# Optimization experiments

Measured on AMD Instinct MI355X. Metric: run time of the kernel, lower is better.

## Reference

```python
import jax, jax.numpy as jnp
import numpy as np

N, E, D = 50000, 800000, 128
BN_EPS = 1e-5


def setup_inputs() -> dict:
    key = jax.random.key(0)
    ks = jax.random.split(key, 6)
    x = jax.random.normal(ks[0], (N, D), dtype=jnp.float32)
    edge_index = jax.random.randint(ks[1], (2, E), 0, N, dtype=jnp.int32)
    edge_attr = jax.random.normal(ks[2], (E, D), dtype=jnp.float32)
    sc = 1.0 / np.sqrt(D).astype(np.float32)
    W1 = jax.random.normal(ks[3], (D, D), dtype=jnp.float32) * sc
    b1 = jnp.zeros((D,), jnp.float32)
    W2 = jax.random.normal(ks[4], (D, D), dtype=jnp.float32) * sc
    b2 = jnp.zeros((D,), jnp.float32)
    bn_w = jnp.ones((D,), jnp.float32)
    bn_b = jnp.zeros((D,), jnp.float32)
    return dict(x=x, edge_index=edge_index, edge_attr=edge_attr,
                W1=W1, b1=b1, W2=W2, b2=b2, bn_w=bn_w, bn_b=bn_b)


def reference(x, edge_index, edge_attr, W1, b1, W2, b2, bn_w, bn_b):
    # GINEConv: aggr_i = sum_{j->i} ReLU(x_j + e_ji); out = MLP((1+eps)*x + aggr), eps=0
    src, dst = edge_index[0], edge_index[1]
    msg = jax.nn.relu(x[src] + edge_attr)                     # [E, D] gather + elementwise
    aggr = jax.ops.segment_sum(msg, dst, num_segments=x.shape[0])  # scatter-add -> [N, D]
    h = x + aggr                                              # (1 + eps) * x, eps = 0
    h = jax.nn.relu(h @ W1 + b1) @ W2 + b2                    # GIN 2-layer MLP
    h = x + h                                                 # dropout(p=0) + residual
    # BatchNorm1d (training-mode batch statistics, biased variance)
    mean = jnp.mean(h, axis=0)
    var = jnp.var(h, axis=0)
    h = (h - mean) * jax.lax.rsqrt(var + BN_EPS) * bn_w + bn_b
    return h
```

## Files before the change

### kernel.cpp

```cpp
#include <hip/hip_runtime.h>
#include <stdint.h>

#define BN_EPS 1e-5f
#define WPAD 136

typedef short s8v __attribute__((ext_vector_type(8)));
typedef float f4v __attribute__((ext_vector_type(4)));

__device__ __forceinline__ float b2f(uint16_t h){
    uint32_t u = ((uint32_t)h) << 16; float f; __builtin_memcpy(&f, &u, 4); return f;
}
__device__ __forceinline__ uint16_t f2b(float f){
    uint32_t u; __builtin_memcpy(&u, &f, 4);
    uint32_t r = (u + 0x7fffu + ((u >> 16) & 1u)) >> 16;
    return (uint16_t)r;
}
__device__ __forceinline__ float lo16(uint32_t v){ return b2f((uint16_t)(v & 0xffffu)); }
__device__ __forceinline__ float hi16(uint32_t v){ return b2f((uint16_t)(v >> 16)); }
__device__ __forceinline__ uint32_t pack2(float a, float b){
    return (uint32_t)f2b(a) | ((uint32_t)f2b(b) << 16);
}

__global__ void k_detect(const uint32_t* __restrict__ xb, int* __restrict__ flag){
    int tid = threadIdx.x;
    uint32_t w = xb[tid];
    float v; __builtin_memcpy(&v, &w, 4);
    float a = fabsf(v);
    bool plaus = (v == 0.0f) || (a > 1e-6f && a < 1e6f);
    unsigned long long m = __ballot(plaus);
    if (tid == 0) flag[0] = (__popcll(m) >= 48) ? 1 : 0;
}

__global__ __launch_bounds__(256) void k_prep(const void* __restrict__ W1, const void* __restrict__ W2,
                                              const void* __restrict__ b1, const void* __restrict__ b2,
                                              const void* __restrict__ bnw, const void* __restrict__ bnb,
                                              const int* __restrict__ flag,
                                              uint16_t* __restrict__ WT1c, uint16_t* __restrict__ WT2c,
                                              float* __restrict__ vecs){
    bool f32 = flag[0] != 0;
    int i = blockIdx.x * 256 + threadIdx.x;
    if (i < 16384){
        int k = i >> 7, n = i & 127;
        float w1 = f32 ? ((const float*)W1)[i] : b2f(((const uint16_t*)W1)[i]);
        float w2 = f32 ? ((const float*)W2)[i] : b2f(((const uint16_t*)W2)[i]);
        WT1c[n * 128 + k] = f2b(w1);
        WT2c[n * 128 + k] = f2b(w2);
    }
    if (i < 128){
        vecs[i]       = f32 ? ((const float*)b1)[i]  : b2f(((const uint16_t*)b1)[i]);
        vecs[128 + i] = f32 ? ((const float*)b2)[i]  : b2f(((const uint16_t*)b2)[i]);
        vecs[256 + i] = f32 ? ((const float*)bnw)[i] : b2f(((const uint16_t*)bnw)[i]);
        vecs[384 + i] = f32 ? ((const float*)bnb)[i] : b2f(((const uint16_t*)bnb)[i]);
    }
}

__global__ void k_hist(const int* __restrict__ dst, int* __restrict__ counts, int E){
    int e = blockIdx.x * 256 + threadIdx.x;
    if (e < E){
        int d = dst[e];
        if (d >= 0) atomicAdd(&counts[d], 1);
    }
}

__global__ __launch_bounds__(1024) void k_scan(int* __restrict__ counts, int* __restrict__ cursor, int N){
    const int T = 1024;
    int tid = threadIdx.x;
    int chunk = (N + T - 1) / T;
    int beg = tid * chunk;
    int end = beg + chunk; if (end > N) end = N;
    int s = 0;
    for (int i = beg; i < end; ++i) s += counts[i];
    __shared__ int sm[T];
    sm[tid] = s; __syncthreads();
    for (int off = 1; off < T; off <<= 1){
        int v = (tid >= off) ? sm[tid - off] : 0;
        __syncthreads();
        sm[tid] += v;
        __syncthreads();
    }
    int run = sm[tid] - s;
    for (int i = beg; i < end; ++i){
        int c = counts[i];
        counts[i] = run; cursor[i] = run;
        run += c;
    }
    if (tid == T - 1){ counts[N] = run; cursor[N] = run; }
}

__global__ void k_scatter(const int* __restrict__ dst, int* __restrict__ cursor,
                          int* __restrict__ perm, int E){
    int e = blockIdx.x * 256 + threadIdx.x;
    if (e < E){
        int d = dst[e];
        if (d >= 0){
            int p = atomicAdd(&cursor[d], 1);
            if (p >= 0 && p < E) perm[p] = e;
        }
    }
}

__global__ __launch_bounds__(256) void k_agg(const void* __restrict__ x,
                                             const void* __restrict__ ea,
                                             const int* __restrict__ src,
                                             const int* __restrict__ offs,
                                             const int* __restrict__ perm,
                                             const int* __restrict__ flag,
                                             uint32_t* __restrict__ h0_2, int N, int E){
    int node = (blockIdx.x << 2) + (threadIdx.x >> 6);
    int lane = threadIdx.x & 63;
    if (node >= N) return;
    bool f32 = flag[0] != 0;
    int beg = offs[node], end = offs[node + 1];
    if (beg < 0) beg = 0;
    if (end > E) end = E;
    float a0 = 0.f, a1 = 0.f;
    if (f32){
        const float2* xf = (const float2*)x;
        const float2* ef = (const float2*)ea;
        for (int p = beg; p < end; ++p){
            int e = perm[p];
            e = e < 0 ? 0 : (e >= E ? E - 1 : e);
            int s = src[e];
            s = s < 0 ? 0 : (s >= N ? N - 1 : s);
            float2 xv = xf[(size_t)s * 64 + lane];
            float2 ev = ef[(size_t)e * 64 + lane];
            a0 += fmaxf(xv.x + ev.x, 0.f);
            a1 += fmaxf(xv.y + ev.y, 0.f);
        }
        float2 xn = xf[(size_t)node * 64 + lane];
        a0 += xn.x; a1 += xn.y;
    } else {
        const uint32_t* x2 = (const uint32_t*)x;
        const uint32_t* e2 = (const uint32_t*)ea;
        for (int p = beg; p < end; ++p){
            int e = perm[p];
            e = e < 0 ? 0 : (e >= E ? E - 1 : e);
            int s = src[e];
            s = s < 0 ? 0 : (s >= N ? N - 1 : s);
            uint32_t xv = x2[(size_t)s * 64 + lane];
            uint32_t ev = e2[(size_t)e * 64 + lane];
            a0 += fmaxf(lo16(xv) + lo16(ev), 0.f);
            a1 += fmaxf(hi16(xv) + hi16(ev), 0.f);
        }
        uint32_t xn = x2[(size_t)node * 64 + lane];
        a0 += lo16(xn); a1 += hi16(xn);
    }
    h0_2[(size_t)node * 64 + lane] = pack2(a0, a1);
}

__global__ __launch_bounds__(256) void k_mlp(const uint16_t* __restrict__ h0,
                                             const uint16_t* __restrict__ WT1,
                                             const uint16_t* __restrict__ WT2,
                                             const float* __restrict__ vecs,
                                             uint16_t* __restrict__ h2out, int N){
    __shared__ uint16_t Ws[128 * WPAD];
    __shared__ uint16_t H1[64 * WPAD];
    int tid = threadIdx.x;
    int lane = tid & 63;
    int w = tid >> 6;
    int r0 = blockIdx.x * 64;
    int mrow = lane & 15;
    int quad = lane >> 4;

    {
        const uint32_t* g = (const uint32_t*)WT1;
        #pragma unroll
        for (int j = 0; j < 32; ++j){
            int u = tid + 256 * j;
            int el = u << 1; int r = el >> 7, c = el & 127;
            *(uint32_t*)&Ws[r * WPAD + c] = g[u];
        }
    }
    __syncthreads();

    int arow = r0 + (w << 4) + mrow;
    int arow_c = arow < N ? arow : N - 1;
    s8v a[4];
    #pragma unroll
    for (int kt = 0; kt < 4; ++kt)
        a[kt] = *(const s8v*)(h0 + (size_t)arow_c * 128 + kt * 32 + quad * 8);

    #pragma unroll
    for (int nt = 0; nt < 8; ++nt){
        f4v acc = {0.f, 0.f, 0.f, 0.f};
        #pragma unroll
        for (int kt = 0; kt < 4; ++kt){
            s8v b = *(const s8v*)&Ws[(nt * 16 + mrow) * WPAD + kt * 32 + quad * 8];
            acc = __builtin_amdgcn_mfma_f32_16x16x32_bf16(a[kt], b, acc, 0, 0, 0);
        }
        int col = nt * 16 + mrow;
        float bias = vecs[col];
        #pragma unroll
        for (int r = 0; r < 4; ++r){
            float v = fmaxf(acc[r] + bias, 0.f);
            int lrow = (w << 4) + quad * 4 + r;
            H1[lrow * WPAD + col] = f2b(v);
        }
    }
    __syncthreads();

    {
        const uint32_t* g = (const uint32_t*)WT2;
        #pragma unroll
        for (int j = 0; j < 32; ++j){
            int u = tid + 256 * j;
            int el = u << 1; int r = el >> 7, c = el & 127;
            *(uint32_t*)&Ws[r * WPAD + c] = g[u];
        }
    }
    __syncthreads();

    s8v a2[4];
    #pragma unroll
    for (int kt = 0; kt < 4; ++kt)
        a2[kt] = *(const s8v*)&H1[((w << 4) + mrow) * WPAD + kt * 32 + quad * 8];

    #pragma unroll
    for (int nt = 0; nt < 8; ++nt){
        f4v acc = {0.f, 0.f, 0.f, 0.f};
        #pragma unroll
        for (int kt = 0; kt < 4; ++kt){
            s8v b = *(const s8v*)&Ws[(nt * 16 + mrow) * WPAD + kt * 32 + quad * 8];
            acc = __builtin_amdgcn_mfma_f32_16x16x32_bf16(a2[kt], b, acc, 0, 0, 0);
        }
        int col = nt * 16 + mrow;
        float bias = vecs[128 + col];
        #pragma unroll
        for (int r = 0; r < 4; ++r){
            int grow = r0 + (w << 4) + quad * 4 + r;
            if (grow < N)
                h2out[(size_t)grow * 128 + col] = f2b(acc[r] + bias);
        }
    }
}

__global__ __launch_bounds__(256) void k_stats(const uint32_t* __restrict__ h2_2,
                                               const void* __restrict__ x,
                                               const int* __restrict__ flag,
                                               float* __restrict__ ssum,
                                               float* __restrict__ ssq, int N){
    bool f32 = flag[0] != 0;
    int tid = threadIdx.x;
    int cp = tid & 63;
    int rl = tid >> 6;
    int rbase = blockIdx.x * 256;
    int rend = rbase + 256; if (rend > N) rend = N;
    float s0 = 0.f, s1 = 0.f, q0 = 0.f, q1 = 0.f;
    for (int r = rbase + rl; r < rend; r += 4){
        uint32_t hv = h2_2[(size_t)r * 64 + cp];
        float x0, x1;
        if (f32){ float2 xv = ((const float2*)x)[(size_t)r * 64 + cp]; x0 = xv.x; x1 = xv.y; }
        else    { uint32_t xv = ((const uint32_t*)x)[(size_t)r * 64 + cp]; x0 = lo16(xv); x1 = hi16(xv); }
        float f0 = lo16(hv) + x0;
        float f1 = hi16(hv) + x1;
        s0 += f0; q0 += f0 * f0;
        s1 += f1; q1 += f1 * f1;
    }
    __shared__ float R[4][256];
    R[0][tid] = s0; R[1][tid] = s1; R[2][tid] = q0; R[3][tid] = q1;
    __syncthreads();
    if (tid < 64){
        for (int g = 1; g < 4; ++g){
            s0 += R[0][tid + 64 * g]; s1 += R[1][tid + 64 * g];
            q0 += R[2][tid + 64 * g]; q1 += R[3][tid + 64 * g];
        }
        atomicAdd(&ssum[2 * tid],     s0);
        atomicAdd(&ssum[2 * tid + 1], s1);
        atomicAdd(&ssq[2 * tid],      q0);
        atomicAdd(&ssq[2 * tid + 1],  q1);
    }
}

__global__ __launch_bounds__(256) void k_norm(void* __restrict__ out,
                                              const uint32_t* __restrict__ h2_2,
                                              const void* __restrict__ x,
                                              const int* __restrict__ flag,
                                              const float* __restrict__ ssum,
                                              const float* __restrict__ ssq,
                                              const float* __restrict__ vecs,
                                              int N, int total2){
    __shared__ float sc[128], sh[128];
    bool f32 = flag[0] != 0;
    int tid = threadIdx.x;
    if (tid < 128){
        float invN = 1.f / (float)N;
        float mean = ssum[tid] * invN;
        float var = ssq[tid] * invN - mean * mean;
        var = fmaxf(var, 0.f);
        float s = vecs[256 + tid] * rsqrtf(var + BN_EPS);
        sc[tid] = s;
        sh[tid] = vecs[384 + tid] - mean * s;
    }
    __syncthreads();
    for (int i = blockIdx.x * 256 + tid; i < total2; i += gridDim.x * 256){
        uint32_t hv = h2_2[i];
        float x0, x1;
        if (f32){ float2 xv = ((const float2*)x)[i]; x0 = xv.x; x1 = xv.y; }
        else    { uint32_t xv = ((const uint32_t*)x)[i]; x0 = lo16(xv); x1 = hi16(xv); }
        int cp = i & 63;
        float f0 = (lo16(hv) + x0) * sc[2 * cp]     + sh[2 * cp];
        float f1 = (hi16(hv) + x1) * sc[2 * cp + 1] + sh[2 * cp + 1];
        if (f32){ float2 o; o.x = f0; o.y = f1; ((float2*)out)[i] = o; }
        else    { ((uint32_t*)out)[i] = pack2(f0, f1); }
    }
}

extern "C" void kernel_launch(void* const* d_in, const int* in_sizes, int n_in,
                              void* d_out, int out_size, void* d_ws, size_t ws_size,
                              hipStream_t stream){
    const void* x   = d_in[0];
    const int*  ei  = (const int*)d_in[1];
    const void* ea  = d_in[2];
    const void* W1  = d_in[3];
    const void* b1  = d_in[4];
    const void* W2  = d_in[5];
    const void* b2  = d_in[6];
    const void* bnw = d_in[7];
    const void* bnb = d_in[8];

    int N = in_sizes[0] / 128;
    int E = in_sizes[1] / 2;
    const int* src = ei;
    const int* dst = ei + E;

    char* ws = (char*)d_ws;
    size_t off = 0;
    auto alloc = [&](size_t bytes){ size_t o = off; off += (bytes + 255) & ~(size_t)255; return o; };
    size_t o_counts = alloc((size_t)(N + 1) * 4);
    size_t o_cursor = alloc((size_t)(N + 1) * 4);
    size_t o_stats  = alloc(256 * 4);
    size_t o_flag   = alloc(4);
    size_t zeroBytes = off;
    size_t o_wt1  = alloc(16384 * 2);
    size_t o_wt2  = alloc(16384 * 2);
    size_t o_vecs = alloc(512 * 4);
    size_t o_h2   = alloc((size_t)N * 128 * 2);
    size_t o_perm = alloc((size_t)E * 4);

    int E_used = E;
    if (off > ws_size){
        size_t fixed = o_perm;
        size_t avail = ws_size > fixed ? ws_size - fixed : 0;
        long long cap = (long long)(avail / 4);
        if (cap < E_used) E_used = (int)(cap < 0 ? 0 : cap);
    }

    int* counts = (int*)(ws + o_counts);
    int* cursor = (int*)(ws + o_cursor);
    float* ssum = (float*)(ws + o_stats);
    float* ssq  = ssum + 128;
    int* flag   = (int*)(ws + o_flag);
    uint16_t* WT1 = (uint16_t*)(ws + o_wt1);
    uint16_t* WT2 = (uint16_t*)(ws + o_wt2);
    float* vecs = (float*)(ws + o_vecs);
    uint16_t* h2 = (uint16_t*)(ws + o_h2);
    int* perm   = (int*)(ws + o_perm);
    uint16_t* h0 = (uint16_t*)d_out;

    hipMemsetAsync(d_ws, 0, zeroBytes, stream);

    k_detect<<<1, 64, 0, stream>>>((const uint32_t*)x, flag);
    k_hist<<<(E_used + 255) / 256, 256, 0, stream>>>(dst, counts, E_used);
    k_scan<<<1, 1024, 0, stream>>>(counts, cursor, N);
    k_scatter<<<(E_used + 255) / 256, 256, 0, stream>>>(dst, cursor, perm, E_used);
    k_prep<<<64, 256, 0, stream>>>(W1, W2, b1, b2, bnw, bnb, flag, WT1, WT2, vecs);
    k_agg<<<(N + 3) / 4, 256, 0, stream>>>(x, ea, src, counts, perm, flag,
                                           (uint32_t*)h0, N, E_used);
    k_mlp<<<(N + 63) / 64, 256, 0, stream>>>(h0, WT1, WT2, vecs, h2, N);
    k_stats<<<(N + 255) / 256, 256, 0, stream>>>((const uint32_t*)h2, x, flag, ssum, ssq, N);
    k_norm<<<2048, 256, 0, stream>>>(d_out, (const uint32_t*)h2, x, flag, ssum, ssq,
                                     vecs, N, N * 64);
}
```

Before: 926.6 us.

## Pack edge/src pairs, batch-load indices in agg, fuse BN stats into MLP

The scatter kernel now writes (edge, src) pairs, so aggregation no longer needs a dependent src lookup. Each wave loads 64 pairs at once and broadcasts them with shuffles, unrolled by four to keep more gathers in flight. The MLP kernel now adds the residual, writes h3 in fp32 and accumulates the BatchNorm sums in shared memory, which removes the separate stats kernel. The cost is an fp32 intermediate that doubles h3 traffic, plus the MLP reading x itself.

```diff
diff --git a/kernel.cpp b/kernel.cpp
--- a/kernel.cpp
+++ b/kernel.cpp
@@ -54,11 +54,11 @@
     }
 }
 
-__global__ void k_hist(const int* __restrict__ dst, int* __restrict__ counts, int E){
+__global__ void k_hist(const int* __restrict__ dst, int* __restrict__ counts, int N, int E){
     int e = blockIdx.x * 256 + threadIdx.x;
     if (e < E){
         int d = dst[e];
-        if (d >= 0) atomicAdd(&counts[d], 1);
+        if (d >= 0 && d < N) atomicAdd(&counts[d], 1);
     }
 }
 
@@ -87,23 +87,25 @@
     if (tid == T - 1){ counts[N] = run; cursor[N] = run; }
 }
 
-__global__ void k_scatter(const int* __restrict__ dst, int* __restrict__ cursor,
-                          int* __restrict__ perm, int E){
+__global__ void k_scatter(const int* __restrict__ dst, const int* __restrict__ src,
+                          int* __restrict__ cursor, int2* __restrict__ pe, int N, int E){
     int e = blockIdx.x * 256 + threadIdx.x;
     if (e < E){
         int d = dst[e];
-        if (d >= 0){
+        if (d >= 0 && d < N){
             int p = atomicAdd(&cursor[d], 1);
-            if (p >= 0 && p < E) perm[p] = e;
+            if (p >= 0 && p < E){
+                int2 v; v.x = e; v.y = src[e];
+                pe[p] = v;
+            }
         }
     }
 }
 
 __global__ __launch_bounds__(256) void k_agg(const void* __restrict__ x,
                                              const void* __restrict__ ea,
-                                             const int* __restrict__ src,
+                                             const int2* __restrict__ pe,
                                              const int* __restrict__ offs,
-                                             const int* __restrict__ perm,
                                              const int* __restrict__ flag,
                                              uint32_t* __restrict__ h0_2, int N, int E){
     int node = (blockIdx.x << 2) + (threadIdx.x >> 6);
@@ -114,35 +116,75 @@
     if (beg < 0) beg = 0;
     if (end > E) end = E;
     float a0 = 0.f, a1 = 0.f;
+
+    const float2* xf = (const float2*)x;
+    const float2* ef = (const float2*)ea;
+    const uint32_t* xh = (const uint32_t*)x;
+    const uint32_t* eh = (const uint32_t*)ea;
+
+    for (int cb = beg; cb < end; cb += 64){
+        int idx = cb + lane;
+        int2 p;
+        if (idx < end) p = pe[idx]; else { p.x = 0; p.y = 0; }
+        int e = p.x, s = p.y;
+        e = e < 0 ? 0 : (e >= E ? E - 1 : e);
+        s = s < 0 ? 0 : (s >= N ? N - 1 : s);
+        int m = end - cb; if (m > 64) m = 64;
+
+        if (f32){
+            int i = 0;
+            for (; i + 4 <= m; i += 4){
+                int e0 = __shfl(e, i),     s0 = __shfl(s, i);
+                int e1 = __shfl(e, i + 1), s1 = __shfl(s, i + 1);
+                int e2 = __shfl(e, i + 2), s2 = __shfl(s, i + 2);
+                int e3 = __shfl(e, i + 3), s3 = __shfl(s, i + 3);
+                float2 x0 = xf[(size_t)s0 * 64 + lane], v0 = ef[(size_t)e0 * 64 + lane];
+                float2 x1 = xf[(size_t)s1 * 64 + lane], v1 = ef[(size_t)e1 * 64 + lane];
+                float2 x2 = xf[(size_t)s2 * 64 + lane], v2 = ef[(size_t)e2 * 64 + lane];
+                float2 x3 = xf[(size_t)s3 * 64 + lane], v3 = ef[(size_t)e3 * 64 + lane];
+                a0 += fmaxf(x0.x + v0.x, 0.f); a1 += fmaxf(x0.y + v0.y, 0.f);
+                a0 += fmaxf(x1.x + v1.x, 0.f); a1 += fmaxf(x1.y + v1.y, 0.f);
+                a0 += fmaxf(x2.x + v2.x, 0.f); a1 += fmaxf(x2.y + v2.y, 0.f);
+                a0 += fmaxf(x3.x + v3.x, 0.f); a1 += fmaxf(x3.y + v3.y, 0.f);
+            }
+            for (; i < m; ++i){
+                int ei = __shfl(e, i), si = __shfl(s, i);
+                float2 xv = xf[(size_t)si * 64 + lane];
+                float2 ev = ef[(size_t)ei * 64 + lane];
+                a0 += fmaxf(xv.x + ev.x, 0.f);
+                a1 += fmaxf(xv.y + ev.y, 0.f);
+            }
+        } else {
+            int i = 0;
+            for (; i + 4 <= m; i += 4){
+                int e0 = __shfl(e, i),     s0 = __shfl(s, i);
+                int e1 = __shfl(e, i + 1), s1 = __shfl(s, i + 1);
+                int e2 = __shfl(e, i + 2), s2 = __shfl(s, i + 2);
+                int e3 = __shfl(e, i + 3), s3 = __shfl(s, i + 3);
+                uint32_t x0 = xh[(size_t)s0 * 64 + lane], v0 = eh[(size_t)e0 * 64 + lane];
+                uint32_t x1 = xh[(size_t)s1 * 64 + lane], v1 = eh[(size_t)e1 * 64 + lane];
+                uint32_t x2 = xh[(size_t)s2 * 64 + lane], v2 = eh[(size_t)e2 * 64 + lane];
+                uint32_t x3 = xh[(size_t)s3 * 64 + lane], v3 = eh[(size_t)e3 * 64 + lane];
+                a0 += fmaxf(lo16(x0) + lo16(v0), 0.f); a1 += fmaxf(hi16(x0) + hi16(v0), 0.f);
+                a0 += fmaxf(lo16(x1) + lo16(v1), 0.f); a1 += fmaxf(hi16(x1) + hi16(v1), 0.f);
+                a0 += fmaxf(lo16(x2) + lo16(v2), 0.f); a1 += fmaxf(hi16(x2) + hi16(v2), 0.f);
+                a0 += fmaxf(lo16(x3) + lo16(v3), 0.f); a1 += fmaxf(hi16(x3) + hi16(v3), 0.f);
+            }
+            for (; i < m; ++i){
+                int ei = __shfl(e, i), si = __shfl(s, i);
+                uint32_t xv = xh[(size_t)si * 64 + lane];
+                uint32_t ev = eh[(size_t)ei * 64 + lane];
+                a0 += fmaxf(lo16(xv) + lo16(ev), 0.f);
+                a1 += fmaxf(hi16(xv) + hi16(ev), 0.f);
+            }
+        }
+    }
+
     if (f32){
-        const float2* xf = (const float2*)x;
-        const float2* ef = (const float2*)ea;
-        for (int p = beg; p < end; ++p){
-            int e = perm[p];
-            e = e < 0 ? 0 : (e >= E ? E - 1 : e);
-            int s = src[e];
-            s = s < 0 ? 0 : (s >= N ? N - 1 : s);
-            float2 xv = xf[(size_t)s * 64 + lane];
-            float2 ev = ef[(size_t)e * 64 + lane];
-            a0 += fmaxf(xv.x + ev.x, 0.f);
-            a1 += fmaxf(xv.y + ev.y, 0.f);
-        }
         float2 xn = xf[(size_t)node * 64 + lane];
         a0 += xn.x; a1 += xn.y;
     } else {
-        const uint32_t* x2 = (const uint32_t*)x;
-        const uint32_t* e2 = (const uint32_t*)ea;
-        for (int p = beg; p < end; ++p){
-            int e = perm[p];
-            e = e < 0 ? 0 : (e >= E ? E - 1 : e);
-            int s = src[e];
-            s = s < 0 ? 0 : (s >= N ? N - 1 : s);
-            uint32_t xv = x2[(size_t)s * 64 + lane];
-            uint32_t ev = e2[(size_t)e * 64 + lane];
-            a0 += fmaxf(lo16(xv) + lo16(ev), 0.f);
-            a1 += fmaxf(hi16(xv) + hi16(ev), 0.f);
-        }
-        uint32_t xn = x2[(size_t)node * 64 + lane];
+        uint32_t xn = xh[(size_t)node * 64 + lane];
         a0 += lo16(xn); a1 += hi16(xn);
     }
     h0_2[(size_t)node * 64 + lane] = pack2(a0, a1);
@@ -152,9 +194,15 @@
                                              const uint16_t* __restrict__ WT1,
                                              const uint16_t* __restrict__ WT2,
                                              const float* __restrict__ vecs,
-                                             uint16_t* __restrict__ h2out, int N){
+                                             const void* __restrict__ x,
+                                             const int* __restrict__ flag,
+                                             float* __restrict__ h3out,
+                                             float* __restrict__ ssum,
+                                             float* __restrict__ ssq, int N){
     __shared__ uint16_t Ws[128 * WPAD];
     __shared__ uint16_t H1[64 * WPAD];
+    __shared__ float lsum[128], lsq[128];
+    bool xf32 = flag[0] != 0;
     int tid = threadIdx.x;
     int lane = tid & 63;
     int w = tid >> 6;
@@ -162,6 +210,8 @@
     int mrow = lane & 15;
     int quad = lane >> 4;
 
+    if (tid < 128){ lsum[tid] = 0.f; lsq[tid] = 0.f; }
+
     {
         const uint32_t* g = (const uint32_t*)WT1;
         #pragma unroll
@@ -215,6 +265,9 @@
     for (int kt = 0; kt < 4; ++kt)
         a2[kt] = *(const s8v*)&H1[((w << 4) + mrow) * WPAD + kt * 32 + quad * 8];
 
+    const float* xf = (const float*)x;
+    const uint16_t* xh = (const uint16_t*)x;
+
     #pragma unroll
     for (int nt = 0; nt < 8; ++nt){
         f4v acc = {0.f, 0.f, 0.f, 0.f};
@@ -225,55 +278,36 @@
         }
         int col = nt * 16 + mrow;
         float bias = vecs[128 + col];
+        float s_part = 0.f, q_part = 0.f;
         #pragma unroll
         for (int r = 0; r < 4; ++r){
             int grow = r0 + (w << 4) + quad * 4 + r;
-            if (grow < N)
-                h2out[(size_t)grow * 128 + col] = f2b(acc[r] + bias);
-        }
-    }
-}
-
-__global__ __launch_bounds__(256) void k_stats(const uint32_t* __restrict__ h2_2,
-                                               const void* __restrict__ x,
-                                               const int* __restrict__ flag,
-                                               float* __restrict__ ssum,
-                                               float* __restrict__ ssq, int N){
-    bool f32 = flag[0] != 0;
-    int tid = threadIdx.x;
-    int cp = tid & 63;
-    int rl = tid >> 6;
-    int rbase = blockIdx.x * 256;
-    int rend = rbase + 256; if (rend > N) rend = N;
-    float s0 = 0.f, s1 = 0.f, q0 = 0.f, q1 = 0.f;
-    for (int r = rbase + rl; r < rend; r += 4){
-        uint32_t hv = h2_2[(size_t)r * 64 + cp];
-        float x0, x1;
-        if (f32){ float2 xv = ((const float2*)x)[(size_t)r * 64 + cp]; x0 = xv.x; x1 = xv.y; }
-        else    { uint32_t xv = ((const uint32_t*)x)[(size_t)r * 64 + cp]; x0 = lo16(xv); x1 = hi16(xv); }
-        float f0 = lo16(hv) + x0;
-        float f1 = hi16(hv) + x1;
-        s0 += f0; q0 += f0 * f0;
-        s1 += f1; q1 += f1 * f1;
-    }
-    __shared__ float R[4][256];
-    R[0][tid] = s0; R[1][tid] = s1; R[2][tid] = q0; R[3][tid] = q1;
+            if (grow < N){
+                float xv = xf32 ? xf[(size_t)grow * 128 + col]
+                                : b2f(xh[(size_t)grow * 128 + col]);
+                float h3 = xv + acc[r] + bias;
+                h3out[(size_t)grow * 128 + col] = h3;
+                s_part += h3; q_part += h3 * h3;
+            }
+        }
+        float sr = s_part + __shfl_xor(s_part, 16);
+        sr += __shfl_xor(sr, 32);
+        float qr = q_part + __shfl_xor(q_part, 16);
+        qr += __shfl_xor(qr, 32);
+        if (quad == 0){
+            atomicAdd(&lsum[col], sr);
+            atomicAdd(&lsq[col], qr);
+        }
+    }
     __syncthreads();
-    if (tid < 64){
-        for (int g = 1; g < 4; ++g){
-            s0 += R[0][tid + 64 * g]; s1 += R[1][tid + 64 * g];
-            q0 += R[2][tid + 64 * g]; q1 += R[3][tid + 64 * g];
-        }
-        atomicAdd(&ssum[2 * tid],     s0);
-        atomicAdd(&ssum[2 * tid + 1], s1);
-        atomicAdd(&ssq[2 * tid],      q0);
-        atomicAdd(&ssq[2 * tid + 1],  q1);
+    if (tid < 128){
+        atomicAdd(&ssum[tid], lsum[tid]);
+        atomicAdd(&ssq[tid], lsq[tid]);
     }
 }
 
 __global__ __launch_bounds__(256) void k_norm(void* __restrict__ out,
-                                              const uint32_t* __restrict__ h2_2,
-                                              const void* __restrict__ x,
+                                              const float2* __restrict__ h3,
                                               const int* __restrict__ flag,
                                               const float* __restrict__ ssum,
                                               const float* __restrict__ ssq,
@@ -293,13 +327,10 @@
     }
     __syncthreads();
     for (int i = blockIdx.x * 256 + tid; i < total2; i += gridDim.x * 256){
-        uint32_t hv = h2_2[i];
-        float x0, x1;
-        if (f32){ float2 xv = ((const float2*)x)[i]; x0 = xv.x; x1 = xv.y; }
-        else    { uint32_t xv = ((const uint32_t*)x)[i]; x0 = lo16(xv); x1 = hi16(xv); }
+        float2 h = h3[i];
         int cp = i & 63;
-        float f0 = (lo16(hv) + x0) * sc[2 * cp]     + sh[2 * cp];
-        float f1 = (hi16(hv) + x1) * sc[2 * cp + 1] + sh[2 * cp + 1];
+        float f0 = h.x * sc[2 * cp]     + sh[2 * cp];
+        float f1 = h.y * sc[2 * cp + 1] + sh[2 * cp + 1];
         if (f32){ float2 o; o.x = f0; o.y = f1; ((float2*)out)[i] = o; }
         else    { ((uint32_t*)out)[i] = pack2(f0, f1); }
     }
@@ -334,14 +365,14 @@
     size_t o_wt1  = alloc(16384 * 2);
     size_t o_wt2  = alloc(16384 * 2);
     size_t o_vecs = alloc(512 * 4);
-    size_t o_h2   = alloc((size_t)N * 128 * 2);
-    size_t o_perm = alloc((size_t)E * 4);
+    size_t o_h3   = alloc((size_t)N * 128 * 4);
+    size_t o_pe   = alloc((size_t)E * 8);
 
     int E_used = E;
     if (off > ws_size){
-        size_t fixed = o_perm;
+        size_t fixed = o_pe;
         size_t avail = ws_size > fixed ? ws_size - fixed : 0;
-        long long cap = (long long)(avail / 4);
+        long long cap = (long long)(avail / 8);
         if (cap < E_used) E_used = (int)(cap < 0 ? 0 : cap);
     }
 
@@ -353,21 +384,20 @@
     uint16_t* WT1 = (uint16_t*)(ws + o_wt1);
     uint16_t* WT2 = (uint16_t*)(ws + o_wt2);
     float* vecs = (float*)(ws + o_vecs);
-    uint16_t* h2 = (uint16_t*)(ws + o_h2);
-    int* perm   = (int*)(ws + o_perm);
+    float* h3   = (float*)(ws + o_h3);
+    int2* pe    = (int2*)(ws + o_pe);
     uint16_t* h0 = (uint16_t*)d_out;
 
     hipMemsetAsync(d_ws, 0, zeroBytes, stream);
 
     k_detect<<<1, 64, 0, stream>>>((const uint32_t*)x, flag);
-    k_hist<<<(E_used + 255) / 256, 256, 0, stream>>>(dst, counts, E_used);
+    k_hist<<<(E_used + 255) / 256, 256, 0, stream>>>(dst, counts, N, E_used);
     k_scan<<<1, 1024, 0, stream>>>(counts, cursor, N);
-    k_scatter<<<(E_used + 255) / 256, 256, 0, stream>>>(dst, cursor, perm, E_used);
+    k_scatter<<<(E_used + 255) / 256, 256, 0, stream>>>(dst, src, cursor, pe, N, E_used);
     k_prep<<<64, 256, 0, stream>>>(W1, W2, b1, b2, bnw, bnb, flag, WT1, WT2, vecs);
-    k_agg<<<(N + 3) / 4, 256, 0, stream>>>(x, ea, src, counts, perm, flag,
+    k_agg<<<(N + 3) / 4, 256, 0, stream>>>(x, ea, pe, counts, flag,
                                            (uint32_t*)h0, N, E_used);
-    k_mlp<<<(N + 63) / 64, 256, 0, stream>>>(h0, WT1, WT2, vecs, h2, N);
-    k_stats<<<(N + 255) / 256, 256, 0, stream>>>((const uint32_t*)h2, x, flag, ssum, ssq, N);
-    k_norm<<<2048, 256, 0, stream>>>(d_out, (const uint32_t*)h2, x, flag, ssum, ssq,
+    k_mlp<<<(N + 63) / 64, 256, 0, stream>>>(h0, WT1, WT2, vecs, x, flag, h3, ssum, ssq, N);
+    k_norm<<<2048, 256, 0, stream>>>(d_out, (const float2*)h3, flag, ssum, ssq,
                                      vecs, N, N * 64);
 }
```

Measured after the change: 839.5 us. -9.4%, faster.
